# Kernel tuning notes

Hardware: AMD Instinct MI355X
Metric: run time of the kernel (lower is better)

The kernel has to match this reference:

```python
import jax, jax.numpy as jnp
import numpy as np

B, S, DIM, H = 2, 2048, 2048, 16
HD = DIM // H  # 128
ROPE_THETA = 10000.0
NEG = -1e9


def setup_inputs() -> dict:
    key = jax.random.key(0)
    ks = jax.random.split(key, 6)
    x = jax.random.normal(ks[0], (B, S, DIM), dtype=jnp.float32)
    # rotary embedding tables: angle[s, j] = s / theta^(2j/HD), j in [0, HD/2)
    inv_freq = 1.0 / (ROPE_THETA ** (jnp.arange(0, HD, 2, dtype=jnp.float32) / HD))
    angles = jnp.arange(S, dtype=jnp.float32)[:, None] * inv_freq[None, :]  # (S, HD/2)
    freqs_cos = jnp.cos(angles)
    freqs_sin = jnp.sin(angles)
    # causal additive mask (1,1,S,S)
    causal = jnp.tril(jnp.ones((S, S), dtype=jnp.bool_))
    mask = jnp.where(causal, 0.0, NEG).astype(jnp.float32)[None, None]
    sc = 1.0 / np.sqrt(DIM)
    wq = jax.random.normal(ks[1], (DIM, DIM), dtype=jnp.float32) * sc
    wk = jax.random.normal(ks[2], (DIM, DIM), dtype=jnp.float32) * sc
    wv = jax.random.normal(ks[3], (DIM, DIM), dtype=jnp.float32) * sc
    wo = jax.random.normal(ks[4], (DIM, DIM), dtype=jnp.float32) * sc
    return {"x": x, "freqs_cos": freqs_cos, "freqs_sin": freqs_sin,
            "mask": mask, "wq": wq, "wk": wk, "wv": wv, "wo": wo}


def _apply_rope(t, cos, sin):
    # t: (B,S,H,HD); cos/sin: (S, HD/2) -> broadcast (1,S,1,HD/2)
    tr = t[..., ::2]
    ti = t[..., 1::2]
    c = cos[None, :, None, :]
    s = sin[None, :, None, :]
    out_r = tr * c - ti * s
    out_i = tr * s + ti * c
    # interleave back: stack on last axis then flatten -> [r0,i0,r1,i1,...]
    return jnp.stack([out_r, out_i], axis=-1).reshape(t.shape)


def reference(x, freqs_cos, freqs_sin, mask, wq, wk, wv, wo):
    b, s, _ = x.shape
    xq = (x @ wq).reshape(b, s, H, HD)
    xk = (x @ wk).reshape(b, s, H, HD)
    xv = (x @ wv).reshape(b, s, H, HD)
    xq = _apply_rope(xq, freqs_cos, freqs_sin)
    xk = _apply_rope(xk, freqs_cos, freqs_sin)
    # (B,H,S,HD)
    q = jnp.transpose(xq, (0, 2, 1, 3)) * (1.0 / np.sqrt(HD))
    k = jnp.transpose(xk, (0, 2, 1, 3))
    v = jnp.transpose(xv, (0, 2, 1, 3))
    attn = jnp.einsum('bhqd,bhkd->bhqk', q, k) + mask[:, :, :s, :s]
    attn = jax.nn.softmax(attn, axis=-1)
    out = jnp.einsum('bhqk,bhkd->bhqd', attn, v)  # (B,H,S,HD)
    out = jnp.transpose(out, (0, 2, 1, 3)).reshape(b, s, H * HD)
    return out @ wo
```

## Files before the change

kernel.cpp:

```cpp
#include <hip/hip_runtime.h>
#include <hip/hip_bf16.h>
#include <cstdint>
#include <cstddef>

#define BB   2
#define SS   2048
#define DD   2048
#define HH   16
#define HDD  128
#define SEC  8388608

typedef unsigned short u16;
typedef __attribute__((ext_vector_type(8))) short short8;
typedef __attribute__((ext_vector_type(4))) float f32x4;

__device__ __forceinline__ u16 f2bf(float f) {
  union { float f; uint32_t u; } v; v.f = f;
  uint32_t r = v.u + 0x7fffu + ((v.u >> 16) & 1u);
  return (u16)(r >> 16);
}
__device__ __forceinline__ float bf2f(u16 b) {
  union { uint32_t u; float f; } v; v.u = ((uint32_t)b) << 16;
  return v.f;
}

__device__ __forceinline__ void gload16(const u16* g, u16* l) {
  __builtin_amdgcn_global_load_lds(
      (__attribute__((address_space(1))) void*)g,
      (__attribute__((address_space(3))) void*)l, 16, 0, 0);
}

__global__ void k_cvt(const float* __restrict__ x, u16* __restrict__ o) {
  int i = blockIdx.x * blockDim.x + threadIdx.x;
  const float4 v = reinterpret_cast<const float4*>(x)[i];
  uint2 p;
  p.x = (uint32_t)f2bf(v.x) | ((uint32_t)f2bf(v.y) << 16);
  p.y = (uint32_t)f2bf(v.z) | ((uint32_t)f2bf(v.w) << 16);
  reinterpret_cast<uint2*>(o)[i] = p;
}

__global__ void k_wt4(const float* __restrict__ w0, const float* __restrict__ w1,
                      const float* __restrict__ w2, const float* __restrict__ w3,
                      u16* __restrict__ wt) {
  __shared__ float t[32][33];
  const int z = blockIdx.z;
  const float* w = (z == 0) ? w0 : (z == 1) ? w1 : (z == 2) ? w2 : w3;
  u16* o = wt + (size_t)z * (DD * DD);
  const int n0 = blockIdx.x * 32, k0 = blockIdx.y * 32;
  const int tx = threadIdx.x, ty = threadIdx.y;
#pragma unroll
  for (int i = 0; i < 32; i += 8)
    t[ty + i][tx] = w[(size_t)(k0 + ty + i) * DD + n0 + tx];
  __syncthreads();
#pragma unroll
  for (int i = 0; i < 32; i += 8)
    o[(size_t)(n0 + ty + i) * DD + k0 + tx] = f2bf(t[tx][ty + i]);
}

__global__ void k_rope(u16* __restrict__ Q, u16* __restrict__ Kb,
                       const float* __restrict__ fc, const float* __restrict__ fs) {
  const int idx = blockIdx.x * blockDim.x + threadIdx.x;
  const int p = idx & 63;
  const int s = (idx >> 6) & (SS - 1);
  const float cv = fc[s * 64 + p], sv = fs[s * 64 + p];
  const size_t off = ((size_t)(idx >> 6)) * HDD + p * 2;
  const float sc = 0.08838834764831845f;
  const float qr = bf2f(Q[off]), qi = bf2f(Q[off + 1]);
  Q[off]      = f2bf((qr * cv - qi * sv) * sc);
  Q[off + 1]  = f2bf((qr * sv + qi * cv) * sc);
  const float kr = bf2f(Kb[off]), ki = bf2f(Kb[off + 1]);
  Kb[off]     = f2bf(kr * cv - ki * sv);
  Kb[off + 1] = f2bf(kr * sv + ki * cv);
}

template <int MODE>
__global__ __launch_bounds__(256) void k_gemm(const u16* __restrict__ A,
                                              const u16* __restrict__ Bt,
                                              void* __restrict__ out) {
  __shared__ __align__(16) u16 As[128 * 32];
  __shared__ __align__(16) u16 Bs[128 * 32];
  const int tid = threadIdx.x;
  const int wave = tid >> 6, lane = tid & 63;
  const int c = lane & 15, g = lane >> 4;
  const int row0 = blockIdx.x * 128, col0 = blockIdx.y * 128;
  const int wm = wave >> 1, wn = wave & 1;
  const int sr = lane >> 2;
  const int sk = (((lane & 3) ^ ((lane >> 3) & 3))) * 8;
  f32x4 acc[4][4] = {};
  for (int k0 = 0; k0 < DD; k0 += 32) {
#pragma unroll
    for (int r = 0; r < 2; ++r) {
      const int chunk = r * 4 + wave;
      const int row = chunk * 16 + sr;
      gload16(A  + (size_t)(row0 + row) * DD + k0 + sk, As + chunk * 512);
      gload16(Bt + (size_t)(col0 + row) * DD + k0 + sk, Bs + chunk * 512);
    }
    __syncthreads();
    short8 a[4], b[4];
    const int gq = (g ^ ((c >> 1) & 3)) * 8;
#pragma unroll
    for (int i = 0; i < 4; ++i)
      a[i] = *reinterpret_cast<const short8*>(As + (wm * 64 + i * 16 + c) * 32 + gq);
#pragma unroll
    for (int j = 0; j < 4; ++j)
      b[j] = *reinterpret_cast<const short8*>(Bs + (wn * 64 + j * 16 + c) * 32 + gq);
#pragma unroll
    for (int i = 0; i < 4; ++i)
#pragma unroll
      for (int j = 0; j < 4; ++j)
        acc[i][j] = __builtin_amdgcn_mfma_f32_16x16x32_bf16(a[i], b[j], acc[i][j], 0, 0, 0);
    __syncthreads();
  }
#pragma unroll
  for (int i = 0; i < 4; ++i) {
#pragma unroll
    for (int j = 0; j < 4; ++j) {
      const int mb = row0 + wm * 64 + i * 16 + g * 4;
      const int n  = col0 + wn * 64 + j * 16 + c;
#pragma unroll
      for (int r = 0; r < 4; ++r) {
        const int m = mb + r;
        if (MODE == 0) {
          const int which = n >> 11;
          const int b_ = m >> 11, s_ = m & (SS - 1);
          const int h_ = (n >> 7) & 15, d_ = n & (HDD - 1);
          size_t idx;
          if (which == 2)
            idx = 2 * (size_t)SEC + (((size_t)(b_ * HH + h_)) * HDD + d_) * SS + s_;
          else
            idx = (size_t)which * SEC + (((size_t)(b_ * HH + h_)) * SS + s_) * HDD + d_;
          reinterpret_cast<u16*>(out)[idx] = f2bf(acc[i][j][r]);
        } else {
          reinterpret_cast<float*>(out)[(size_t)m * DD + n] = acc[i][j][r];
        }
      }
    }
  }
}

__global__ __launch_bounds__(256, 3) void k_attn(const u16* __restrict__ Q,
                                                 const u16* __restrict__ K,
                                                 const u16* __restrict__ Vt,
                                                 u16* __restrict__ O) {
  __shared__ __align__(16) u16 Kt[2][32 * 128];
  __shared__ __align__(16) u16 Vs[2][128 * 32];
  __shared__ __align__(16) u16 Pb[4 * 32 * 40];
  const int tid = threadIdx.x;
  const int wave = tid >> 6, lane = tid & 63;
  const int c = lane & 15, g = lane >> 4;
  const int l = blockIdx.x;
  int qi, bh;
  if (l < 256) { qi = 8 + (l & 7); bh = l >> 3; }
  else         { qi = 7 - ((l - 256) & 7); bh = (l - 256) >> 3; }
  const int q0 = qi * 128;
  const u16* Qp = Q  + (size_t)bh * SS * HDD;
  const u16* Kp = K  + (size_t)bh * SS * HDD;
  const u16* Vp = Vt + (size_t)bh * SS * HDD;
  short8 qf[2][4];
#pragma unroll
  for (int ms = 0; ms < 2; ++ms)
#pragma unroll
    for (int kd = 0; kd < 4; ++kd)
      qf[ms][kd] = *reinterpret_cast<const short8*>(
          Qp + (size_t)(q0 + wave * 32 + ms * 16 + c) * HDD + kd * 32 + g * 8);
  f32x4 acc[2][8] = {};
  float psum[2][4] = {};
  const int ntiles = (qi + 1) * 4;
  u16* pwav = Pb + wave * (32 * 40);
  const int krl = lane >> 4, kcl = lane & 15;
  const int vrl = lane >> 2, vcl = lane & 3;
  auto stage = [&](int t) {
    const int kv0 = t * 32;
    u16* kb = Kt[t & 1];
    u16* vb = Vs[t & 1];
#pragma unroll
    for (int j = 0; j < 2; ++j) {
      const int r0k = (j * 4 + wave) * 4;
      const int rowk = r0k + krl;
      gload16(Kp + (size_t)(kv0 + rowk) * HDD + ((kcl ^ (rowk & 15)) << 3),
              kb + r0k * 128);
      const int r0v = (j * 4 + wave) * 16;
      const int rowv = r0v + vrl;
      gload16(Vp + (size_t)rowv * SS + kv0 + ((vcl ^ (vrl & 3)) << 3),
              vb + r0v * 32);
    }
  };
  stage(0);
  for (int t = 0; t < ntiles; ++t) {
    __syncthreads();
    if (t + 1 < ntiles) stage(t + 1);
    const int kv0 = t * 32;
    const bool active = kv0 <= q0 + wave * 32 + 31;
    if (!active) continue;
    const u16* kb = Kt[t & 1];
    const u16* vv = Vs[t & 1];
    f32x4 s[2][2] = {};
#pragma unroll
    for (int ns = 0; ns < 2; ++ns)
#pragma unroll
      for (int kd = 0; kd < 4; ++kd) {
        const short8 b = *reinterpret_cast<const short8*>(
            kb + (ns * 16 + c) * 128 + (((kd * 4 + g) ^ c) << 3));
        s[0][ns] = __builtin_amdgcn_mfma_f32_16x16x32_bf16(qf[0][kd], b, s[0][ns], 0, 0, 0);
        s[1][ns] = __builtin_amdgcn_mfma_f32_16x16x32_bf16(qf[1][kd], b, s[1][ns], 0, 0, 0);
      }
#pragma unroll
    for (int ms = 0; ms < 2; ++ms) {
      const int qrow = q0 + wave * 32 + ms * 16 + g * 4;
#pragma unroll
      for (int r = 0; r < 4; ++r) {
        u16* pw = pwav + (ms * 16 + g * 4 + r) * 40 + c;
        float rs = 0.f;
#pragma unroll
        for (int ns = 0; ns < 2; ++ns) {
          const bool u = (kv0 + ns * 16 + c) <= (qrow + r);
          const float p = u ? __expf(s[ms][ns][r]) : 0.f;
          rs += p;
          pw[ns * 16] = f2bf(p);
        }
        psum[ms][r] += rs;
      }
    }
    short8 pa[2];
    pa[0] = *reinterpret_cast<const short8*>(pwav + c * 40 + g * 8);
    pa[1] = *reinterpret_cast<const short8*>(pwav + (16 + c) * 40 + g * 8);
#pragma unroll
    for (int nb = 0; nb < 8; ++nb) {
      const short8 vb2 = *reinterpret_cast<const short8*>(
          vv + (nb * 16 + c) * 32 + ((g ^ (c & 3)) << 3));
      acc[0][nb] = __builtin_amdgcn_mfma_f32_16x16x32_bf16(pa[0], vb2, acc[0][nb], 0, 0, 0);
      acc[1][nb] = __builtin_amdgcn_mfma_f32_16x16x32_bf16(pa[1], vb2, acc[1][nb], 0, 0, 0);
    }
  }
  const int b_ = bh >> 4, h_ = bh & 15;
#pragma unroll
  for (int ms = 0; ms < 2; ++ms) {
#pragma unroll
    for (int r = 0; r < 4; ++r) {
      float rs = psum[ms][r];
      rs += __shfl_xor(rs, 1);
      rs += __shfl_xor(rs, 2);
      rs += __shfl_xor(rs, 4);
      rs += __shfl_xor(rs, 8);
      const float inv = 1.f / rs;
      const int s_ = q0 + wave * 32 + ms * 16 + g * 4 + r;
      u16* op = O + ((size_t)(b_ * SS + s_)) * DD + h_ * HDD;
#pragma unroll
      for (int nb = 0; nb < 8; ++nb)
        op[nb * 16 + c] = f2bf(acc[ms][nb][r] * inv);
    }
  }
}

extern "C" void kernel_launch(void* const* d_in, const int* in_sizes, int n_in,
                              void* d_out, int out_size, void* d_ws, size_t ws_size,
                              hipStream_t stream) {
  const float* x  = (const float*)d_in[0];
  const float* fc = (const float*)d_in[1];
  const float* fs = (const float*)d_in[2];
  const float* wq = (const float*)d_in[4];
  const float* wk = (const float*)d_in[5];
  const float* wv = (const float*)d_in[6];
  const float* wo = (const float*)d_in[7];

  u16* ws  = (u16*)d_ws;
  u16* xb  = ws;
  u16* wqt = xb  + 8388608;
  u16* wot = wqt + 3 * 4194304;
  u16* Qb  = wot + 4194304;
  u16* Kb  = Qb  + SEC;
  u16* Vtb = Kb  + SEC;
  u16* ao  = Vtb + SEC;

  k_cvt<<<8192, 256, 0, stream>>>(x, xb);
  k_wt4<<<dim3(64, 64, 4), dim3(32, 8), 0, stream>>>(wq, wk, wv, wo, wqt);
  k_gemm<0><<<dim3(32, 48), 256, 0, stream>>>(xb, wqt, (void*)Qb);
  k_rope<<<16384, 256, 0, stream>>>(Qb, Kb, fc, fs);
  k_attn<<<512, 256, 0, stream>>>(Qb, Kb, Vtb, ao);
  k_gemm<1><<<dim3(32, 16), 256, 0, stream>>>(ao, wot, d_out);
}
```

Measured before the change: 450.9 us.

## Fuse RoPE into QKV GEMM epilogue and merge conversion kernels

Merges the x conversion and weight transpose kernels into one launch, and applies RoPE plus query scaling directly in the QKV GEMM epilogue using a lane shuffle to fetch the paired element. This removes the separate RoPE kernel's read and write of Q and K. The V-transpose store is vectorized to 4-element packed writes. The LDS XOR swizzle in the GEMM is also removed, which may reintroduce bank conflicts on the shared-memory fragment reads.

```diff
diff --git a/kernel.cpp b/kernel.cpp
--- a/kernel.cpp
+++ b/kernel.cpp
@@ -30,53 +30,47 @@
       (__attribute__((address_space(3))) void*)l, 16, 0, 0);
 }
 
-__global__ void k_cvt(const float* __restrict__ x, u16* __restrict__ o) {
-  int i = blockIdx.x * blockDim.x + threadIdx.x;
-  const float4 v = reinterpret_cast<const float4*>(x)[i];
-  uint2 p;
-  p.x = (uint32_t)f2bf(v.x) | ((uint32_t)f2bf(v.y) << 16);
-  p.y = (uint32_t)f2bf(v.z) | ((uint32_t)f2bf(v.w) << 16);
-  reinterpret_cast<uint2*>(o)[i] = p;
-}
-
-__global__ void k_wt4(const float* __restrict__ w0, const float* __restrict__ w1,
-                      const float* __restrict__ w2, const float* __restrict__ w3,
-                      u16* __restrict__ wt) {
-  __shared__ float t[32][33];
+__global__ void k_prep(const float* __restrict__ x,
+                       const float* __restrict__ w0, const float* __restrict__ w1,
+                       const float* __restrict__ w2, const float* __restrict__ w3,
+                       u16* __restrict__ xb, u16* __restrict__ wt) {
   const int z = blockIdx.z;
+  if (z == 4) {
+    const int id = blockIdx.y * 64 + blockIdx.x;
+    const int t = threadIdx.y * 32 + threadIdx.x;
+    const size_t base = ((size_t)id * 256 + t) * 2;
+    const float4* xv = reinterpret_cast<const float4*>(x);
+    uint2* ov = reinterpret_cast<uint2*>(xb);
+#pragma unroll
+    for (int u = 0; u < 2; ++u) {
+      const float4 v = xv[base + u];
+      uint2 p;
+      p.x = (uint32_t)f2bf(v.x) | ((uint32_t)f2bf(v.y) << 16);
+      p.y = (uint32_t)f2bf(v.z) | ((uint32_t)f2bf(v.w) << 16);
+      ov[base + u] = p;
+    }
+    return;
+  }
+  __shared__ float tls[32][33];
   const float* w = (z == 0) ? w0 : (z == 1) ? w1 : (z == 2) ? w2 : w3;
   u16* o = wt + (size_t)z * (DD * DD);
   const int n0 = blockIdx.x * 32, k0 = blockIdx.y * 32;
   const int tx = threadIdx.x, ty = threadIdx.y;
 #pragma unroll
   for (int i = 0; i < 32; i += 8)
-    t[ty + i][tx] = w[(size_t)(k0 + ty + i) * DD + n0 + tx];
+    tls[ty + i][tx] = w[(size_t)(k0 + ty + i) * DD + n0 + tx];
   __syncthreads();
 #pragma unroll
   for (int i = 0; i < 32; i += 8)
-    o[(size_t)(n0 + ty + i) * DD + k0 + tx] = f2bf(t[tx][ty + i]);
-}
-
-__global__ void k_rope(u16* __restrict__ Q, u16* __restrict__ Kb,
-                       const float* __restrict__ fc, const float* __restrict__ fs) {
-  const int idx = blockIdx.x * blockDim.x + threadIdx.x;
-  const int p = idx & 63;
-  const int s = (idx >> 6) & (SS - 1);
-  const float cv = fc[s * 64 + p], sv = fs[s * 64 + p];
-  const size_t off = ((size_t)(idx >> 6)) * HDD + p * 2;
-  const float sc = 0.08838834764831845f;
-  const float qr = bf2f(Q[off]), qi = bf2f(Q[off + 1]);
-  Q[off]      = f2bf((qr * cv - qi * sv) * sc);
-  Q[off + 1]  = f2bf((qr * sv + qi * cv) * sc);
-  const float kr = bf2f(Kb[off]), ki = bf2f(Kb[off + 1]);
-  Kb[off]     = f2bf(kr * cv - ki * sv);
-  Kb[off + 1] = f2bf(kr * sv + ki * cv);
+    o[(size_t)(n0 + ty + i) * DD + k0 + tx] = f2bf(tls[tx][ty + i]);
 }
 
 template <int MODE>
 __global__ __launch_bounds__(256) void k_gemm(const u16* __restrict__ A,
                                               const u16* __restrict__ Bt,
-                                              void* __restrict__ out) {
+                                              void* __restrict__ out,
+                                              const float* __restrict__ fc,
+                                              const float* __restrict__ fs) {
   __shared__ __align__(16) u16 As[128 * 32];
   __shared__ __align__(16) u16 Bs[128 * 32];
   const int tid = threadIdx.x;
@@ -85,7 +79,7 @@
   const int row0 = blockIdx.x * 128, col0 = blockIdx.y * 128;
   const int wm = wave >> 1, wn = wave & 1;
   const int sr = lane >> 2;
-  const int sk = (((lane & 3) ^ ((lane >> 3) & 3))) * 8;
+  const int sk = (lane & 3) * 8;
   f32x4 acc[4][4] = {};
   for (int k0 = 0; k0 < DD; k0 += 32) {
 #pragma unroll
@@ -97,13 +91,12 @@
     }
     __syncthreads();
     short8 a[4], b[4];
-    const int gq = (g ^ ((c >> 1) & 3)) * 8;
 #pragma unroll
     for (int i = 0; i < 4; ++i)
-      a[i] = *reinterpret_cast<const short8*>(As + (wm * 64 + i * 16 + c) * 32 + gq);
+      a[i] = *reinterpret_cast<const short8*>(As + (wm * 64 + i * 16 + c) * 32 + g * 8);
 #pragma unroll
     for (int j = 0; j < 4; ++j)
-      b[j] = *reinterpret_cast<const short8*>(Bs + (wn * 64 + j * 16 + c) * 32 + gq);
+      b[j] = *reinterpret_cast<const short8*>(Bs + (wn * 64 + j * 16 + c) * 32 + g * 8);
 #pragma unroll
     for (int i = 0; i < 4; ++i)
 #pragma unroll
@@ -111,28 +104,50 @@
         acc[i][j] = __builtin_amdgcn_mfma_f32_16x16x32_bf16(a[i], b[j], acc[i][j], 0, 0, 0);
     __syncthreads();
   }
-#pragma unroll
-  for (int i = 0; i < 4; ++i) {
-#pragma unroll
-    for (int j = 0; j < 4; ++j) {
-      const int mb = row0 + wm * 64 + i * 16 + g * 4;
-      const int n  = col0 + wn * 64 + j * 16 + c;
-#pragma unroll
-      for (int r = 0; r < 4; ++r) {
-        const int m = mb + r;
-        if (MODE == 0) {
-          const int which = n >> 11;
-          const int b_ = m >> 11, s_ = m & (SS - 1);
-          const int h_ = (n >> 7) & 15, d_ = n & (HDD - 1);
-          size_t idx;
-          if (which == 2)
-            idx = 2 * (size_t)SEC + (((size_t)(b_ * HH + h_)) * HDD + d_) * SS + s_;
-          else
-            idx = (size_t)which * SEC + (((size_t)(b_ * HH + h_)) * SS + s_) * HDD + d_;
-          reinterpret_cast<u16*>(out)[idx] = f2bf(acc[i][j][r]);
+  if (MODE == 0) {
+    const int which = col0 >> 11;
+    u16* o16 = reinterpret_cast<u16*>(out);
+#pragma unroll
+    for (int i = 0; i < 4; ++i) {
+#pragma unroll
+      for (int j = 0; j < 4; ++j) {
+        const int mb = row0 + wm * 64 + i * 16 + g * 4;
+        const int n  = col0 + wn * 64 + j * 16 + c;
+        const int h_ = (n >> 7) & 15, d_ = n & (HDD - 1);
+        const int b_ = mb >> 11, s0_ = mb & (SS - 1);
+        if (which == 2) {
+          ushort4 pk;
+          pk.x = f2bf(acc[i][j][0]); pk.y = f2bf(acc[i][j][1]);
+          pk.z = f2bf(acc[i][j][2]); pk.w = f2bf(acc[i][j][3]);
+          *reinterpret_cast<ushort4*>(
+              o16 + 2 * (size_t)SEC + (((size_t)(b_ * HH + h_)) * HDD + d_) * SS + s0_) = pk;
         } else {
-          reinterpret_cast<float*>(out)[(size_t)m * DD + n] = acc[i][j][r];
+          const int p = d_ >> 1;
+          const bool ev = (d_ & 1) == 0;
+          const float qsc = (which == 0) ? 0.08838834764831845f : 1.0f;
+#pragma unroll
+          for (int r = 0; r < 4; ++r) {
+            const int s_ = s0_ + r;
+            const float own = acc[i][j][r];
+            const float par = __shfl_xor(own, 1);
+            const float cv = fc[s_ * 64 + p], sv = fs[s_ * 64 + p];
+            const float ro = ev ? (own * cv - par * sv) : (par * sv + own * cv);
+            o16[(size_t)which * SEC + (((size_t)(b_ * HH + h_)) * SS + s_) * HDD + d_] =
+                f2bf(ro * qsc);
+          }
         }
+      }
+    }
+  } else {
+#pragma unroll
+    for (int i = 0; i < 4; ++i) {
+#pragma unroll
+      for (int j = 0; j < 4; ++j) {
+        const int mb = row0 + wm * 64 + i * 16 + g * 4;
+        const int n  = col0 + wn * 64 + j * 16 + c;
+#pragma unroll
+        for (int r = 0; r < 4; ++r)
+          reinterpret_cast<float*>(out)[(size_t)(mb + r) * DD + n] = acc[i][j][r];
       }
     }
   }
@@ -272,10 +287,8 @@
   u16* Vtb = Kb  + SEC;
   u16* ao  = Vtb + SEC;
 
-  k_cvt<<<8192, 256, 0, stream>>>(x, xb);
-  k_wt4<<<dim3(64, 64, 4), dim3(32, 8), 0, stream>>>(wq, wk, wv, wo, wqt);
-  k_gemm<0><<<dim3(32, 48), 256, 0, stream>>>(xb, wqt, (void*)Qb);
-  k_rope<<<16384, 256, 0, stream>>>(Qb, Kb, fc, fs);
+  k_prep<<<dim3(64, 64, 5), dim3(32, 8), 0, stream>>>(x, wq, wk, wv, wo, xb, wqt);
+  k_gemm<0><<<dim3(32, 48), 256, 0, stream>>>(xb, wqt, (void*)Qb, fc, fs);
   k_attn<<<512, 256, 0, stream>>>(Qb, Kb, Vtb, ao);
-  k_gemm<1><<<dim3(32, 16), 256, 0, stream>>>(ao, wot, d_out);
-}
+  k_gemm<1><<<dim3(32, 16), 256, 0, stream>>>(ao, wot, d_out, nullptr, nullptr);
+}
```

Result: faster. 434.6 us (-3.6%).
